# Performance work log

Measured on AMD Instinct MI355X. Metric: run time of the kernel, lower is better.

## Reference

```python
import jax, jax.numpy as jnp
import numpy as np

H = 32      # num_attention_heads
HD = 64     # head_dim
MD = 64     # qk_mqa_dim (rope dim)
EPS = 1e-6
SCALING = (HD + MD) ** -0.5
NEG = -1e9


def rms_norm(x, w):
    var = jnp.mean(jnp.square(x), axis=-1, keepdims=True)
    return x * jax.lax.rsqrt(var + EPS) * w


def rotate_half(x):
    x1, x2 = jnp.split(x, 2, axis=-1)
    return jnp.concatenate([-x2, x1], axis=-1)


def apply_rope(x, cos, sin):
    return x * cos + rotate_half(x) * sin


def setup_inputs() -> dict:
    key = jax.random.key(0)
    ks = jax.random.split(key, 6)
    B, S, D = 1, 2048, 2048
    QR, KVR = 1024, 896
    hidden_states = jax.random.normal(ks[0], (B, S, D), jnp.float32)
    # real rotary tables for the MD-dim rope subspace
    inv_freq = 1.0 / (10000.0 ** (np.arange(0, MD, 2, dtype=np.float32) / MD))
    freqs = np.arange(S, dtype=np.float32)[:, None] * inv_freq[None, :]
    emb = np.concatenate([freqs, freqs], axis=-1)  # [S, MD]
    cos = jnp.asarray(np.cos(emb), jnp.float32)
    sin = jnp.asarray(np.sin(emb), jnp.float32)
    s = 0.02
    Wqa = jax.random.normal(ks[1], (QR, D), jnp.float32) * s
    q_ln_w = jnp.ones((QR,), jnp.float32)
    Wqb = jax.random.normal(ks[2], (H * (HD + MD), QR), jnp.float32) * s
    Wkva = jax.random.normal(ks[3], (KVR + MD, D), jnp.float32) * s
    kv_ln_w = jnp.ones((KVR,), jnp.float32)
    Wkvb = jax.random.normal(ks[4], (2 * H * HD, KVR), jnp.float32) * s
    Wo = jax.random.normal(ks[5], (D, H * HD), jnp.float32) * s
    return {"hidden_states": hidden_states, "cos": cos, "sin": sin,
            "Wqa": Wqa, "q_ln_w": q_ln_w, "Wqb": Wqb,
            "Wkva": Wkva, "kv_ln_w": kv_ln_w, "Wkvb": Wkvb, "Wo": Wo}


def reference(hidden_states, cos, sin, Wqa, q_ln_w, Wqb, Wkva, kv_ln_w, Wkvb, Wo):
    B, S, D = hidden_states.shape
    KVR = kv_ln_w.shape[0]
    # Q: LoRA down -> RMSNorm -> up (weights pre-absorbed with rope split)
    q = rms_norm(hidden_states @ Wqa.T, q_ln_w) @ Wqb.T      # [B,S,H*(HD+MD)]
    q = q.reshape(B, S, H, HD + MD).transpose(0, 2, 1, 3)     # [B,H,S,HD+MD]
    q_nope, q_rope = q[..., :HD], q[..., HD:]
    # KV: shared compressed latent + MQA rope key
    ckv = hidden_states @ Wkva.T                               # [B,S,KVR+MD]
    kv_nope, k_rope = ckv[..., :KVR], ckv[..., KVR:]
    kv_nope = rms_norm(kv_nope, kv_ln_w)
    q_rope = apply_rope(q_rope, cos[None, None], sin[None, None])
    k_rope = apply_rope(k_rope[:, None], cos[None, None], sin[None, None])  # [B,1,S,MD]
    # up-project latent to per-head K_nope and V (interleaved per head)
    kv = (kv_nope @ Wkvb.T).reshape(B, S, H, 2 * HD).transpose(0, 2, 1, 3)  # [B,H,S,2*HD]
    k_nope, value = kv[..., :HD], kv[..., HD:]
    key_states = jnp.concatenate(
        [k_nope, jnp.broadcast_to(k_rope, (B, H, S, MD))], axis=-1)  # repeat_kv of rope part
    query_states = jnp.concatenate([q_nope, q_rope], axis=-1)        # [B,H,S,HD+MD]
    # causal SDPA with scaling = (head_dim + qk_mqa_dim)^-0.5
    scores = jnp.einsum('bhqd,bhkd->bhqk', query_states, key_states) * SCALING
    causal = jnp.tril(jnp.ones((S, S), bool))
    scores = jnp.where(causal[None, None], scores, NEG)
    probs = jax.nn.softmax(scores, axis=-1)
    out = jnp.einsum('bhqk,bhkd->bhqd', probs, value)                # [B,H,S,HD]
    out = out.transpose(0, 2, 1, 3).reshape(B, S, H * HD)
    return out @ Wo.T
```

## Files before the change

### kernel.cpp

```cpp
#include <hip/hip_runtime.h>
#include <stdint.h>

typedef unsigned short u16;
typedef __attribute__((ext_vector_type(4))) float f32x4;
typedef __attribute__((ext_vector_type(4))) unsigned short u16x4;
typedef __attribute__((ext_vector_type(8))) unsigned short u16x8;
typedef __attribute__((ext_vector_type(8))) short s16x8;
typedef __attribute__((ext_vector_type(4))) short s16x4;
typedef __attribute__((ext_vector_type(2))) unsigned int u32x2;

#define DEVI static __device__ __forceinline__

#define VMCNT(n) asm volatile("s_waitcnt vmcnt(" #n ")" ::: "memory")
#define SBAR() __builtin_amdgcn_s_barrier()
#define SCHED0() __builtin_amdgcn_sched_barrier(0)

DEVI u16 f2b(float f) {
  union { float f; unsigned u; } v; v.f = f;
  unsigned r = v.u + 0x7fffu + ((v.u >> 16) & 1u);
  return (u16)(r >> 16);
}
DEVI float b2f(u16 b) {
  union { unsigned u; float f; } v; v.u = ((unsigned)b) << 16;
  return v.f;
}

DEVI void gload_lds16(const void* gptr, void* lptr) {
  typedef const __attribute__((address_space(1))) unsigned gq;
  typedef __attribute__((address_space(3))) unsigned lq;
  __builtin_amdgcn_global_load_lds((gq*)(uintptr_t)gptr,
                                   (lq*)(uint32_t)(uintptr_t)lptr, 16, 0, 0);
}

DEVI unsigned cvtpk(float a, float b) {
  unsigned d;
  asm("v_cvt_pk_bf16_f32 %0, %1, %2" : "=v"(d) : "v"(a), "v"(b));
  return d;
}
DEVI f32x4 mfma16(s16x4 a, s16x4 b, f32x4 c) {
  f32x4 d;
  asm("v_mfma_f32_16x16x16_bf16 %0, %1, %2, %3" : "=v"(d) : "v"(a), "v"(b), "v"(c));
  return d;
}
DEVI float exp2a(float x) {
  float d;
  asm("v_exp_f32 %0, %1" : "=v"(d) : "v"(x));
  return d;
}

__global__ __launch_bounds__(256) void cvt_all(
    const float* __restrict__ X, const float* __restrict__ Wqa,
    const float* __restrict__ Wkva, const float* __restrict__ Wqb,
    const float* __restrict__ Wkvb, const float* __restrict__ Wo,
    u16* __restrict__ Xb, u16* __restrict__ W1, u16* __restrict__ Wqbb,
    u16* __restrict__ Wkvbb, u16* __restrict__ Wob) {
  int i = blockIdx.x * 256 + threadIdx.x;
  const int stride = gridDim.x * 256;
  for (; i < 5079040; i += stride) {
    const float* s; u16* d; int j;
    if (i < 1572864) {
      if (i < 1048576) { s = X; d = Xb; j = i; }
      else             { s = Wqa; d = W1; j = i - 1048576; }
    } else if (i < 3112960) {
      if (i < 2064384) { s = Wkva; d = W1 + 1024 * 2048; j = i - 1572864; }
      else             { s = Wqb; d = Wqbb; j = i - 2064384; }
    } else {
      if (i < 4030464) { s = Wkvb; d = Wkvbb; j = i - 3112960; }
      else             { s = Wo; d = Wob; j = i - 4030464; }
    }
    f32x4 v = *(const f32x4*)(s + (size_t)j * 4);
    u16x4 o;
    o[0] = f2b(v[0]); o[1] = f2b(v[1]); o[2] = f2b(v[2]); o[3] = f2b(v[3]);
    *(u16x4*)(d + (size_t)j * 4) = o;
  }
}

#define GEMM_STAGE(AP, BP, KK, k0, buf)                                        \
  {                                                                            \
    _Pragma("unroll") for (int p = 0; p < 4; ++p) {                            \
      const int c = tid + p * 256;                                             \
      const int row = c >> 3, j = c & 7;                                       \
      gload_lds16(AP + (size_t)(m0 + row) * (KK) + (k0) + ((j ^ (row & 7)) * 8), \
                  &As[buf][c * 8]);                                            \
    }                                                                          \
    _Pragma("unroll") for (int p = 0; p < 4; ++p) {                            \
      const int c = tid + p * 256;                                             \
      const int row = c >> 3, j = c & 7;                                       \
      gload_lds16(BP + (size_t)(n0 + row) * (KK) + (k0) + ((j ^ (row & 7)) * 8), \
                  &Bs[buf][c * 8]);                                            \
    }                                                                          \
  }

#define GEMM_COMPUTE(cur)                                                      \
  _Pragma("unroll") for (int kk = 0; kk < 64; kk += 32) {                      \
    s16x8 af[4], bfr[4];                                                       \
    _Pragma("unroll") for (int i = 0; i < 4; ++i) {                            \
      const int rA = wm * 64 + i * 16 + c15;                                   \
      af[i] = *(const s16x8*)((const char*)&As[cur][0] + rA * 128 +            \
                              (((kk + g * 8) * 2) ^ ((rA & 7) << 4)));         \
    }                                                                          \
    _Pragma("unroll") for (int i = 0; i < 4; ++i) {                            \
      const int rB = wn * 64 + i * 16 + c15;                                   \
      bfr[i] = *(const s16x8*)((const char*)&Bs[cur][0] + rB * 128 +           \
                               (((kk + g * 8) * 2) ^ ((rB & 7) << 4)));        \
    }                                                                          \
    _Pragma("unroll") for (int i = 0; i < 4; ++i)                              \
      _Pragma("unroll") for (int j = 0; j < 4; ++j)                            \
        acc[i][j] = __builtin_amdgcn_mfma_f32_16x16x32_bf16(af[i], bfr[j],     \
                                                            acc[i][j], 0, 0, 0); \
  }

#define GEMM_PROLOG                                                            \
  const int tid = threadIdx.x;                                                 \
  const int lane = tid & 63, w = tid >> 6;                                     \
  const int wm = w >> 1, wn = w & 1;                                           \
  const int c15 = lane & 15, g = lane >> 4;                                    \
  const int m0 = blockIdx.y * 128, n0 = blockIdx.x * 128;                      \
  f32x4 acc[4][4] = {};

#define GEMM_LOOP(AP, BP, KK)                                                  \
  GEMM_STAGE(AP, BP, KK, 0, 0);                                                \
  const int nk = (KK) >> 6;                                                    \
  for (int kt = 0; kt < nk; ++kt) {                                            \
    const int cur = kt & 1;                                                    \
    if (kt + 1 < nk) {                                                         \
      GEMM_STAGE(AP, BP, KK, (kt + 1) << 6, cur ^ 1);                          \
      VMCNT(8);                                                                \
    } else {                                                                   \
      VMCNT(0);                                                                \
    }                                                                          \
    SBAR();                                                                    \
    SCHED0();                                                                  \
    GEMM_COMPUTE(cur);                                                         \
    SBAR();                                                                    \
    SCHED0();                                                                  \
  }

template <int OUT_BF16>
__global__ __launch_bounds__(256) void gemm_out(const u16* __restrict__ A,
                                                const u16* __restrict__ B,
                                                void* __restrict__ Cv,
                                                int M, int N, int K) {
  __shared__ __align__(16) u16 As[2][128 * 64];
  __shared__ __align__(16) u16 Bs[2][128 * 64];
  GEMM_PROLOG
  GEMM_LOOP(A, B, K)
#pragma unroll
  for (int i = 0; i < 4; ++i)
#pragma unroll
    for (int j = 0; j < 4; ++j) {
      const int mr = m0 + wm * 64 + i * 16 + g * 4;
      const int nc = n0 + wn * 64 + j * 16 + c15;
#pragma unroll
      for (int r = 0; r < 4; ++r) {
        if (OUT_BF16)
          ((u16*)Cv)[(size_t)(mr + r) * N + nc] = f2b(acc[i][j][r]);
        else
          ((float*)Cv)[(size_t)(mr + r) * N + nc] = acc[i][j][r];
      }
    }
}

__global__ __launch_bounds__(256) void gemm2_fused(
    const u16* __restrict__ qn, const u16* __restrict__ Wqbb,
    const u16* __restrict__ kvn, const u16* __restrict__ Wkvbb,
    u16* __restrict__ qraw, char* __restrict__ KbB, char* __restrict__ VtB) {
  __shared__ __align__(16) u16 As[2][128 * 64];
  __shared__ __align__(16) u16 Bs[2][128 * 64];
  const int z = blockIdx.z;
  const u16* A = z ? kvn : qn;
  const u16* B = z ? Wkvbb : Wqbb;
  const int K = z ? 896 : 1024;
  GEMM_PROLOG
  GEMM_LOOP(A, B, K)

  if (z == 0) {
#pragma unroll
    for (int i = 0; i < 4; ++i)
#pragma unroll
      for (int j = 0; j < 4; ++j) {
        const int mr = m0 + wm * 64 + i * 16 + g * 4;
        const int nc = n0 + wn * 64 + j * 16 + c15;
#pragma unroll
        for (int r = 0; r < 4; ++r)
          qraw[(size_t)(mr + r) * 4096 + nc] = f2b(acc[i][j][r]);
      }
  } else {
    const int h = n0 >> 7;
#pragma unroll
    for (int i = 0; i < 4; ++i)
#pragma unroll
      for (int j = 0; j < 4; ++j) {
        const int mr = m0 + wm * 64 + i * 16 + g * 4;
        if (wn == 0) {
          const int d = j * 16 + c15;
#pragma unroll
          for (int r = 0; r < 4; ++r) {
            const int s = mr + r;
            *(u16*)(KbB + ((size_t)(h * 2048 + s) << 8) +
                    ((2 * d) ^ ((s & 7) << 4))) = f2b(acc[i][j][r]);
          }
        } else {
          const int d = j * 16 + c15;
          u16x4 o;
#pragma unroll
          for (int r = 0; r < 4; ++r) o[r] = f2b(acc[i][j][r]);
          *(u16x4*)(VtB + ((size_t)(h * 64 + d) << 12) +
                    ((2 * mr) ^ ((d & 7) << 4))) = o;
        }
      }
  }
}

DEVI float block_sum(float v, float* sbuf, int tid) {
#pragma unroll
  for (int o = 32; o; o >>= 1) v += __shfl_xor(v, o, 64);
  __syncthreads();
  if ((tid & 63) == 0) sbuf[tid >> 6] = v;
  __syncthreads();
  return sbuf[0] + sbuf[1] + sbuf[2] + sbuf[3];
}

__global__ __launch_bounds__(256) void norm_rope(const u16* __restrict__ C1b,
    const float* __restrict__ qw, const float* __restrict__ kw,
    const float* __restrict__ cosb, const float* __restrict__ sinb,
    u16* __restrict__ qn, u16* __restrict__ kvn, char* __restrict__ KbB) {
  __shared__ float sbuf[4];
  __shared__ __align__(16) u16 rv[64];
  const int s = blockIdx.x, tid = threadIdx.x;
  const u16* row = C1b + (size_t)s * 2048;

  u16x4 qv4 = *(const u16x4*)(row + tid * 4);
  float q0 = b2f(qv4[0]), q1 = b2f(qv4[1]), q2 = b2f(qv4[2]), q3 = b2f(qv4[3]);
  float ss = q0*q0 + q1*q1 + q2*q2 + q3*q3;
  ss = block_sum(ss, sbuf, tid);
  const float scale = rsqrtf(ss * (1.f / 1024.f) + 1e-6f);
  {
    f32x4 wv = *(const f32x4*)(qw + tid * 4);
    u16x4 o;
    o[0] = f2b(q0 * scale * wv[0]); o[1] = f2b(q1 * scale * wv[1]);
    o[2] = f2b(q2 * scale * wv[2]); o[3] = f2b(q3 * scale * wv[3]);
    *(u16x4*)(qn + (size_t)s * 1024 + tid * 4) = o;
  }

  float ss2 = 0.f;
  float k0 = 0, k1 = 0, k2 = 0, k3 = 0;
  if (tid < 224) {
    u16x4 kv4 = *(const u16x4*)(row + 1024 + tid * 4);
    k0 = b2f(kv4[0]); k1 = b2f(kv4[1]); k2 = b2f(kv4[2]); k3 = b2f(kv4[3]);
    ss2 = k0*k0 + k1*k1 + k2*k2 + k3*k3;
  }
  ss2 = block_sum(ss2, sbuf, tid);
  const float sc2 = rsqrtf(ss2 * (1.f / 896.f) + 1e-6f);
  if (tid < 224) {
    f32x4 wv = *(const f32x4*)(kw + tid * 4);
    u16x4 o;
    o[0] = f2b(k0 * sc2 * wv[0]); o[1] = f2b(k1 * sc2 * wv[1]);
    o[2] = f2b(k2 * sc2 * wv[2]); o[3] = f2b(k3 * sc2 * wv[3]);
    *(u16x4*)(kvn + (size_t)s * 896 + tid * 4) = o;
  }

  if (tid < 64) {
    const int d = tid;
    const float x = b2f(row[1920 + d]);
    const float part = b2f(row[1920 + (d < 32 ? d + 32 : d - 32)]);
    const float cv = cosb[s * 64 + d], sv = sinb[s * 64 + d];
    rv[d] = f2b(d < 32 ? (x * cv - part * sv) : (x * cv + part * sv));
  }
  __syncthreads();
  {
    const int h = tid >> 3, c8 = tid & 7;
    const u16x8 v = *(const u16x8*)&rv[c8 * 8];
    *(u16x8*)(KbB + ((size_t)(h * 2048 + s) << 8) +
              ((128 + c8 * 16) ^ ((s & 7) << 4))) = v;
  }
}

__global__ __launch_bounds__(256) void attn_fwd(
    const u16* __restrict__ Qb, const u16* __restrict__ Kb,
    const u16* __restrict__ Vt, const float* __restrict__ cosb,
    const float* __restrict__ sinb, u16* __restrict__ attn) {
  __shared__ __align__(16) u16 Klds[2][64 * 128];
  __shared__ __align__(16) u16 Vlds[2][64 * 64];
  const int tid = threadIdx.x;
  const int lane = tid & 63, w = tid >> 6;
  const int c15 = lane & 15, g = lane >> 4;
  const int orig = blockIdx.x;
  const int xcd = orig & 7, l = orig >> 3;
  const int h = xcd * 4 + (l & 3);
  const int qb = 15 - (l >> 2);
  const int wmin = qb * 128 + w * 32;
  const int wmax = wmin + 31;
  const char* KbHB = (const char*)Kb + ((size_t)h << 19);
  const char* VtHB = (const char*)Vt + ((size_t)h << 18);
  const float SC2 = 0.12753860478587782f;

  s16x8 qf[2][4];
#pragma unroll
  for (int qa = 0; qa < 2; ++qa) {
    const int qrow = wmin + qa * 16 + c15;
    const u16* qp = Qb + (size_t)qrow * 4096 + h * 128;
    u16x8 x0 = *(const u16x8*)(qp + g * 8);
    u16x8 x1 = *(const u16x8*)(qp + 32 + g * 8);
    u16x8 x2 = *(const u16x8*)(qp + 64 + g * 8);
    u16x8 x3 = *(const u16x8*)(qp + 96 + g * 8);
    const float* cb = cosb + (size_t)qrow * 64 + g * 8;
    const float* sb = sinb + (size_t)qrow * 64 + g * 8;
#pragma unroll
    for (int i = 0; i < 8; ++i) {
      qf[qa][0][i] = (short)f2b(b2f(x0[i]) * SC2);
      qf[qa][1][i] = (short)f2b(b2f(x1[i]) * SC2);
      const float f2 = b2f(x2[i]), f3 = b2f(x3[i]);
      qf[qa][2][i] = (short)f2b((f2 * cb[i] - f3 * sb[i]) * SC2);
      qf[qa][3][i] = (short)f2b((f3 * cb[32 + i] + f2 * sb[32 + i]) * SC2);
    }
  }

  const int nt = 2 * qb + 2;
  auto STAGE = [&](int t, int buf) {
    const int kv0 = t << 6;
#pragma unroll
    for (int p = 0; p < 4; ++p) {
      const int c = tid + p * 256;
      gload_lds16(KbHB + ((size_t)(kv0 + (c >> 4)) << 8) + (c & 15) * 16,
                  (char*)Klds[buf] + c * 16);
    }
#pragma unroll
    for (int p = 0; p < 2; ++p) {
      const int c = tid + p * 256;
      gload_lds16(VtHB + ((size_t)(c >> 3) << 12) + 2 * kv0 + (c & 7) * 16,
                  (char*)Vlds[buf] + c * 16);
    }
  };

  f32x4 acc[2][4] = {};
  float m[2] = {-1e9f, -1e9f}, ssum[2] = {0.f, 0.f};

  STAGE(0, 0);

  for (int t = 0; t < nt; ++t) {
    const int cur = t & 1;
    const int kv0 = t << 6;
    if (t + 1 < nt) {
      STAGE(t + 1, cur ^ 1);
      VMCNT(6);
    } else {
      VMCNT(0);
    }
    SBAR();
    SCHED0();

    if (kv0 <= wmax) {
      const u16* Kc = Klds[cur];
      const u16* Vc = Vlds[cur];

      float pv[2][4][4];
      __builtin_amdgcn_s_setprio(1);
#pragma unroll
      for (int kvh = 0; kvh < 4; ++kvh) {
        s16x8 kf[4];
        const int rb = (kvh * 16 + c15) * 256;
#pragma unroll
        for (int d0 = 0; d0 < 4; ++d0)
          kf[d0] = *(const s16x8*)((const char*)Kc + rb +
                                   ((d0 * 64 + g * 16) ^ ((c15 & 7) << 4)));
#pragma unroll
        for (int qa = 0; qa < 2; ++qa) {
          f32x4 s4 = {};
#pragma unroll
          for (int d0 = 0; d0 < 4; ++d0)
            s4 = __builtin_amdgcn_mfma_f32_16x16x32_bf16(kf[d0], qf[qa][d0], s4, 0, 0, 0);
          pv[qa][kvh][0] = s4[0]; pv[qa][kvh][1] = s4[1];
          pv[qa][kvh][2] = s4[2]; pv[qa][kvh][3] = s4[3];
        }
      }
      __builtin_amdgcn_s_setprio(0);

      if (kv0 + 63 > wmin) {
#pragma unroll
        for (int qa = 0; qa < 2; ++qa) {
          const int qrow = wmin + qa * 16 + c15;
#pragma unroll
          for (int kvh = 0; kvh < 4; ++kvh)
#pragma unroll
            for (int r = 0; r < 4; ++r) {
              const int kv = kv0 + kvh * 16 + g * 4 + r;
              if (kv > qrow) pv[qa][kvh][r] = -1e9f;
            }
        }
      }

      s16x4 pB[2][4];
#pragma unroll
      for (int qa = 0; qa < 2; ++qa) {
        float pm = -1e9f;
#pragma unroll
        for (int kvh = 0; kvh < 4; ++kvh)
#pragma unroll
          for (int r = 0; r < 4; ++r) pm = fmaxf(pm, pv[qa][kvh][r]);
        pm = fmaxf(pm, __shfl_xor(pm, 16, 64));
        pm = fmaxf(pm, __shfl_xor(pm, 32, 64));
        if (!__all(pm - m[qa] <= 8.f)) {
          const float mnew = fmaxf(m[qa], pm);
          const float alpha = exp2a(m[qa] - mnew);
          ssum[qa] *= alpha;
#pragma unroll
          for (int dt = 0; dt < 4; ++dt) acc[qa][dt] *= alpha;
          m[qa] = mnew;
        }
#pragma unroll
        for (int kvh = 0; kvh < 4; ++kvh)
#pragma unroll
          for (int r = 0; r < 4; ++r) {
            const float p = exp2a(pv[qa][kvh][r] - m[qa]);
            pv[qa][kvh][r] = p;
            ssum[qa] += p;
          }
#pragma unroll
        for (int ks = 0; ks < 4; ++ks) {
          u32x2 pw;
          pw[0] = cvtpk(pv[qa][ks][0], pv[qa][ks][1]);
          pw[1] = cvtpk(pv[qa][ks][2], pv[qa][ks][3]);
          pB[qa][ks] = __builtin_bit_cast(s16x4, pw);
        }
      }

      __builtin_amdgcn_s_setprio(1);
#pragma unroll
      for (int dt = 0; dt < 4; ++dt) {
        const int rb2 = (dt * 16 + c15) * 128;
#pragma unroll
        for (int ks = 0; ks < 4; ++ks) {
          s16x4 vf = *(const s16x4*)((const char*)Vc + rb2 +
                                     ((ks * 32 + g * 8) ^ ((c15 & 7) << 4)));
          acc[0][dt] = mfma16(vf, pB[0][ks], acc[0][dt]);
          acc[1][dt] = mfma16(vf, pB[1][ks], acc[1][dt]);
        }
      }
      __builtin_amdgcn_s_setprio(0);
    }
    SBAR();
    SCHED0();
  }

#pragma unroll
  for (int qa = 0; qa < 2; ++qa) {
    float sv = ssum[qa];
    sv += __shfl_xor(sv, 16, 64);
    sv += __shfl_xor(sv, 32, 64);
    const float inv = 1.f / sv;
    const int qrow = wmin + qa * 16 + c15;
#pragma unroll
    for (int dt = 0; dt < 4; ++dt) {
      u16x4 o;
#pragma unroll
      for (int r = 0; r < 4; ++r) o[r] = f2b(acc[qa][dt][r] * inv);
      *(u16x4*)(attn + (size_t)qrow * 2048 + h * 64 + dt * 16 + g * 4) = o;
    }
  }
}

extern "C" void kernel_launch(void* const* d_in, const int* in_sizes, int n_in,
                              void* d_out, int out_size, void* d_ws, size_t ws_size,
                              hipStream_t stream) {
  const float* X    = (const float*)d_in[0];
  const float* cosb = (const float*)d_in[1];
  const float* sinb = (const float*)d_in[2];
  const float* Wqa  = (const float*)d_in[3];
  const float* qlnw = (const float*)d_in[4];
  const float* Wqb  = (const float*)d_in[5];
  const float* Wkva = (const float*)d_in[6];
  const float* klnw = (const float*)d_in[7];
  const float* Wkvb = (const float*)d_in[8];
  const float* Wo   = (const float*)d_in[9];
  float* out = (float*)d_out;
  char* ws = (char*)d_ws;

  u16*   Xb     = (u16*)(ws + 0);
  u16*   W1     = (u16*)(ws + 8388608);
  u16*   C1b    = (u16*)(ws + 16777216);
  u16*   qn     = (u16*)(ws + 33554432);
  u16*   kvn    = (u16*)(ws + 37748736);
  u16*   Wqbb   = (u16*)(ws + 41943040);
  u16*   Wkvbb  = (u16*)(ws + 50331648);
  u16*   qraw_b = (u16*)(ws + 0);
  u16*   Kb     = (u16*)(ws + 58720256);
  u16*   VtG    = (u16*)(ws + 75497472);
  u16*   attnb  = (u16*)(ws + 83886080);
  u16*   Wob    = (u16*)(ws + 92274688);

  cvt_all<<<2048, 256, 0, stream>>>(X, Wqa, Wkva, Wqb, Wkvb, Wo,
                                    Xb, W1, Wqbb, Wkvbb, Wob);

  gemm_out<1><<<dim3(16, 16), 256, 0, stream>>>(Xb, W1, C1b, 2048, 2048, 2048);

  norm_rope<<<2048, 256, 0, stream>>>(C1b, qlnw, klnw, cosb, sinb, qn, kvn, (char*)Kb);

  gemm2_fused<<<dim3(32, 16, 2), 256, 0, stream>>>(qn, Wqbb, kvn, Wkvbb,
                                                   qraw_b, (char*)Kb, (char*)VtG);

  attn_fwd<<<512, 256, 0, stream>>>(qraw_b, Kb, VtG, cosb, sinb, attnb);

  gemm_out<0><<<dim3(16, 16), 256, 0, stream>>>(attnb, Wob, out, 2048, 2048, 2048);
}
```

Before: 174.6 us.

## Triple-buffer GEMM K-loop and reorder attention query-block dispatch

The generic gemm_out kernel moves from double to triple buffering in LDS, prefetching two K tiles ahead and waiting on a deeper vmcnt so global loads overlap compute better. LDS use rises to 96KB per block, which may lower occupancy. Separately, the attention block-to-query-block mapping changes so the second half of blocks processes small (early) query blocks in ascending order rather than continuing descending, altering causal load balance.

```diff
diff --git a/kernel.cpp b/kernel.cpp
--- a/kernel.cpp
+++ b/kernel.cpp
@@ -129,11 +129,30 @@
     } else {                                                                   \
       VMCNT(0);                                                                \
     }                                                                          \
-    SBAR();                                                                    \
-    SCHED0();                                                                  \
+    SBAR(); SCHED0();                                                          \
     GEMM_COMPUTE(cur);                                                         \
-    SBAR();                                                                    \
-    SCHED0();                                                                  \
+    SBAR(); SCHED0();                                                          \
+  }
+
+#define GEMM_LOOP3(AP, BP, KK)                                                 \
+  GEMM_STAGE(AP, BP, KK, 0, 0);                                                \
+  GEMM_STAGE(AP, BP, KK, 64, 1);                                               \
+  const int nk = (KK) >> 6;                                                    \
+  int bufc = 0;                                                                \
+  for (int kt = 0; kt < nk; ++kt) {                                            \
+    const int nxt = (bufc + 2 >= 3) ? bufc - 1 : bufc + 2;                     \
+    if (kt + 2 < nk) {                                                         \
+      GEMM_STAGE(AP, BP, KK, (kt + 2) << 6, nxt);                              \
+      VMCNT(16);                                                               \
+    } else if (kt + 1 < nk) {                                                  \
+      VMCNT(8);                                                                \
+    } else {                                                                   \
+      VMCNT(0);                                                                \
+    }                                                                          \
+    SBAR(); SCHED0();                                                          \
+    GEMM_COMPUTE(bufc);                                                        \
+    SBAR(); SCHED0();                                                          \
+    bufc = (bufc + 1 == 3) ? 0 : bufc + 1;                                     \
   }
 
 template <int OUT_BF16>
@@ -141,10 +160,10 @@
                                                 const u16* __restrict__ B,
                                                 void* __restrict__ Cv,
                                                 int M, int N, int K) {
-  __shared__ __align__(16) u16 As[2][128 * 64];
-  __shared__ __align__(16) u16 Bs[2][128 * 64];
+  __shared__ __align__(16) u16 As[3][128 * 64];
+  __shared__ __align__(16) u16 Bs[3][128 * 64];
   GEMM_PROLOG
-  GEMM_LOOP(A, B, K)
+  GEMM_LOOP3(A, B, K)
 #pragma unroll
   for (int i = 0; i < 4; ++i)
 #pragma unroll
@@ -288,7 +307,8 @@
   const int orig = blockIdx.x;
   const int xcd = orig & 7, l = orig >> 3;
   const int h = xcd * 4 + (l & 3);
-  const int qb = 15 - (l >> 2);
+  const int x = l >> 2;
+  const int qb = (x < 8) ? (15 - x) : (x - 8);
   const int wmin = qb * 128 + w * 32;
   const int wmax = wmin + 31;
   const char* KbHB = (const char*)Kb + ((size_t)h << 19);
```

After: 172.8 us. No clear change (-1.0%).
